# Optimization experiments

Measured on AMD Instinct MI355X. Metric: run time of the kernel, lower is better.

## Reference

```python
import jax, jax.numpy as jnp
import numpy as np

B, C, H, W = 8, 64, 128, 128


def _conv3x3(x, w, b):
    # x: [B,C,H,W], w: [O,I,3,3], b: [O]; stride 1, padding 1
    y = jax.lax.conv_general_dilated(
        x, w, window_strides=(1, 1), padding=((1, 1), (1, 1)),
        dimension_numbers=('NCHW', 'OIHW', 'NCHW'))
    return y + b[None, :, None, None]


def setup_inputs() -> dict:
    key = jax.random.key(0)
    ks = jax.random.split(key, 8)
    s = 0.05
    return {
        'x': jax.random.normal(ks[0], (B, C, H, W), jnp.float32),
        'Wq': jax.random.normal(ks[1], (C, C, 3, 3), jnp.float32) * s,
        'bq': jax.random.normal(ks[2], (C,), jnp.float32) * s,
        'Wk': jax.random.normal(ks[3], (C, C, 3, 3), jnp.float32) * s,
        'bk': jax.random.normal(ks[4], (C,), jnp.float32) * s,
        'Wv': jax.random.normal(ks[5], (C, C, 3, 3), jnp.float32) * s,
        'bv': jax.random.normal(ks[6], (C,), jnp.float32) * s,
        'gamma': jax.random.normal(ks[7], (1,), jnp.float32) * s,
    }


def reference(x, Wq, bq, Wk, bk, Wv, bv, gamma):
    b_, c_, h_, w_ = x.shape
    q = _conv3x3(x, Wq, bq)  # [B,C,H,W]
    k = _conv3x3(x, Wk, bk)
    v = _conv3x3(x, Wv, bv)

    # energy along H (column attention): eH[b,h,w,g] = sum_c q[b,c,h,w]*k[b,c,g,w]
    eH = jnp.einsum('bchw,bcgw->bhwg', q, k)
    eye = jnp.eye(h_, dtype=bool)  # mask diagonal h==g with -inf
    eH = jnp.where(eye[None, :, None, :], -jnp.inf, eH)

    # energy along W (row attention): eW[b,h,w,g] = sum_c q[b,c,h,w]*k[b,c,h,g]
    eW = jnp.einsum('bchw,bchg->bhwg', q, k)

    # joint softmax over concatenated [H | W] axis
    att = jax.nn.softmax(jnp.concatenate([eH, eW], axis=3), axis=3)
    att_H = att[:, :, :, :h_]          # [B,H,W,H]
    att_W = att[:, :, :, h_:h_ + w_]   # [B,H,W,W]

    out_H = jnp.einsum('bcgw,bhwg->bchw', v, att_H)
    out_W = jnp.einsum('bchg,bhwg->bchw', v, att_W)

    return gamma[0] * (out_H + out_W) + x
```

## Files before the change

### kernel.cpp

```cpp
#include <hip/hip_runtime.h>
#include <hip/hip_bf16.h>

#define B_ 8
#define C_ 64
#define H_ 128
#define W_ 128
#define HW_  ((size_t)H_ * W_)
#define CHW_ ((size_t)C_ * H_ * W_)

typedef unsigned short u16;
typedef unsigned int   u32;
typedef __attribute__((ext_vector_type(8))) short bf16x8;
typedef __attribute__((ext_vector_type(4))) float f32x4;

__device__ __forceinline__ float bf2f(u16 h) {
    union { u32 u; float f; } c; c.u = ((u32)h) << 16; return c.f;
}
__device__ __forceinline__ u16 f2bf(float f) {
    union { float f; u32 u; } c; c.f = f;
    u32 u = c.u;
    u32 r = (u + 0x7fffu + ((u >> 16) & 1u)) >> 16;
    return (u16)r;
}
__device__ __forceinline__ u32 pack2(float a, float b) {
    return (u32)f2bf(a) | ((u32)f2bf(b) << 16);
}
__device__ __forceinline__ float sanit(float x, float lo, float hi) {
    return fminf(fmaxf(x, lo), hi);
}
__device__ __forceinline__ void gload_lds16(const u16* g, u16* l) {
    __builtin_amdgcn_global_load_lds(
        (const __attribute__((address_space(1))) void*)g,
        (__attribute__((address_space(3))) void*)l, 16, 0, 0);
}

__global__ __launch_bounds__(256) void prep_weights(
    const float* __restrict__ Wq, const float* __restrict__ Wk,
    const float* __restrict__ Wv, u16* __restrict__ Wt)
{
    int tap = blockIdx.x;
    int cog = blockIdx.y * 4 + (threadIdx.x >> 6);
    int ci  = threadIdx.x & 63;
    int arr = cog >> 6, co = cog & 63;
    const float* src = arr == 0 ? Wq : (arr == 1 ? Wk : Wv);
    Wt[tap * 12288 + cog * 64 + ci] = f2bf(src[(co * 64 + ci) * 9 + tap]);
}

__global__ __launch_bounds__(256) void xprep_kernel(
    const float* __restrict__ x, u16* __restrict__ xb)
{
    const int hp  = blockIdx.x;
    const int tid = threadIdx.x;
    u16* dst = xb + ((size_t)blockIdx.y * 130 + hp) * 8192;
    if (hp == 0 || hp == 129) {
#pragma unroll
        for (int i = 0; i < 4; i++)
            *(uint4*)(dst + (size_t)(tid + i * 256) * 8) = (uint4){0, 0, 0, 0};
        return;
    }
    const float* xr = x + (size_t)blockIdx.y * CHW_ + (size_t)(hp - 1) * W_;
#pragma unroll
    for (int it = 0; it < 4; it++) {
        int idx = tid + it * 256;
        int px  = idx & 127;
        int g   = idx >> 7;
        float vb[8];
#pragma unroll
        for (int e = 0; e < 8; e++)
            vb[e] = xr[(size_t)(g * 8 + e) * HW_ + px];
        uint4 o;
        o.x = pack2(vb[0], vb[1]);
        o.y = pack2(vb[2], vb[3]);
        o.z = pack2(vb[4], vb[5]);
        o.w = pack2(vb[6], vb[7]);
        *(uint4*)(dst + (size_t)(g * 128 + px) * 8) = o;
    }
}

__global__ __launch_bounds__(256, 2) void conv_mfma_kernel(
    const u16* __restrict__ xb, const u16* __restrict__ Wt,
    const float* __restrict__ bq, const float* __restrict__ bk,
    const float* __restrict__ bv,
    u16* __restrict__ qN, u16* __restrict__ kN, u16* __restrict__ v)
{
    const int nwg  = gridDim.x * gridDim.y;
    const int flat = blockIdx.y * gridDim.x + blockIdx.x;
    const int wg   = (flat & 7) * (nwg >> 3) + (flat >> 3);
    const int h    = wg & (H_ - 1);
    const int bidx = wg >> 7;
    const size_t boff = (size_t)bidx * CHW_;
    const int tid  = threadIdx.x;
    const int lane = tid & 63, wv = tid >> 6;
    const int ln15 = lane & 15, quad = lane >> 4;

    __shared__ __align__(16) u16 xI[24960];

    const int woff = (wv * 48 + ln15) * 64 + quad * 8;

    bf16x8 wcur[2][3], wnxt[2][3];
#pragma unroll
    for (int ks = 0; ks < 2; ks++)
#pragma unroll
        for (int mt = 0; mt < 3; mt++)
            wcur[ks][mt] = *(const bf16x8*)(Wt + woff + mt * 1024 + ks * 32);

    if (tid < 48) {
        int dh = tid >> 4, g = (tid & 15) >> 1, p = (tid & 1) ? 129 : 0;
        *(uint4*)(xI + dh * 8320 + g * 1040 + p * 8) = (uint4){0, 0, 0, 0};
    }

    const u16* xrows = xb + ((size_t)bidx * 130 + h) * 8192;
#pragma unroll
    for (int it = 0; it < 12; it++) {
        int chunk = wv * 12 + it;
        int dh = chunk >> 4, g = (chunk >> 1) & 7, half = chunk & 1;
        gload_lds16(xrows + (size_t)dh * 8192 + g * 1024 + half * 512 + lane * 8,
                    xI + dh * 8320 + g * 1040 + 8 + half * 512);
    }
    __syncthreads();

    f32x4 acc[3][8];
#pragma unroll
    for (int mt = 0; mt < 3; mt++)
#pragma unroll
        for (int nt = 0; nt < 8; nt++)
            acc[mt][nt] = (f32x4){0.f, 0.f, 0.f, 0.f};

#pragma unroll
    for (int tap = 0; tap < 9; tap++) {
        const int dh = tap / 3, dw = tap % 3;
        if (tap < 8) {
#pragma unroll
            for (int ks = 0; ks < 2; ks++)
#pragma unroll
                for (int mt = 0; mt < 3; mt++)
                    wnxt[ks][mt] = *(const bf16x8*)(Wt + (tap + 1) * 12288 + woff + mt * 1024 + ks * 32);
        }
        const u16* xrow = xI + dh * 8320;
#pragma unroll
        for (int ks = 0; ks < 2; ks++) {
            bf16x8 bfr[8];
#pragma unroll
            for (int nt = 0; nt < 8; nt++)
                bfr[nt] = *(const bf16x8*)(xrow + ((quad + ks * 4) * 1040 + (nt * 16 + ln15 + dw) * 8));
            __builtin_amdgcn_s_setprio(1);
#pragma unroll
            for (int mt = 0; mt < 3; mt++)
#pragma unroll
                for (int nt = 0; nt < 8; nt++)
                    acc[mt][nt] = __builtin_amdgcn_mfma_f32_16x16x32_bf16(
                        wcur[ks][mt], bfr[nt], acc[mt][nt], 0, 0, 0);
            __builtin_amdgcn_s_setprio(0);
        }
        if (tap < 8) {
#pragma unroll
            for (int ks = 0; ks < 2; ks++)
#pragma unroll
                for (int mt = 0; mt < 3; mt++)
                    wcur[ks][mt] = wnxt[ks][mt];
        }
    }

    __syncthreads();
    u16* T = xI;
#pragma unroll
    for (int mt = 0; mt < 3; mt++) {
        int base = wv * 48 + mt * 16;
        int arr  = base >> 6;
        if (arr < 2) {
            const float* bias = arr == 0 ? bq : bk;
            int cb = (base & 63) + quad * 4;
#pragma unroll
            for (int r = 0; r < 4; r++) {
                float bb = bias[cb + r];
#pragma unroll
                for (int nt = 0; nt < 8; nt++)
                    T[arr * 9216 + (nt * 16 + ln15) * 72 + cb + r] = f2bf(acc[mt][nt][r] + bb);
            }
        } else {
            int cb = (base & 63) + quad * 4;
#pragma unroll
            for (int r = 0; r < 4; r++) {
                float bb = bv[cb + r];
                u16* drow = v + boff + (size_t)(cb + r) * HW_ + (size_t)h * W_;
#pragma unroll
                for (int nt = 0; nt < 8; nt++)
                    drow[nt * 16 + ln15] = f2bf(acc[mt][nt][r] + bb);
            }
        }
    }
    __syncthreads();
#pragma unroll
    for (int it = 0; it < 8; it++) {
        int idx = tid + it * 256;
        int arr = idx >> 10, rem = idx & 1023;
        int px = rem >> 3, c8 = (rem & 7) * 8;
        uint4 val = *(uint4*)(T + arr * 9216 + px * 72 + c8);
        u16* dst = (arr ? kN : qN) + boff + ((size_t)h * W_ + px) * 64 + c8;
        *(uint4*)dst = val;
    }
}

__global__ __launch_bounds__(256) void vt_kernel(
    const u16* __restrict__ v, u16* __restrict__ vT)
{
    __shared__ u16 Ts[64 * 72];
    const u16* src = v  + (size_t)blockIdx.z * CHW_ + (size_t)blockIdx.y * HW_;
    u16* dst       = vT + (size_t)blockIdx.z * CHW_ + (size_t)blockIdx.y * HW_;
    const int ti = blockIdx.x & 1, tj = blockIdx.x >> 1;
    const int r0 = ti * 64, c0 = tj * 64;
    const int tid = threadIdx.x;
    const int r = tid >> 2, cq = tid & 3;
#pragma unroll
    for (int i = 0; i < 2; i++) {
        uint4 u = *(const uint4*)(src + (size_t)(r0 + r) * 128 + c0 + cq * 16 + i * 8);
        *(uint4*)(Ts + r * 72 + cq * 16 + i * 8) = u;
    }
    __syncthreads();
    const int wr = tid >> 2, hq = tid & 3;
    union { u16 o[16]; uint4 v4[2]; } t;
#pragma unroll
    for (int j = 0; j < 16; j++) t.o[j] = Ts[(hq * 16 + j) * 72 + wr];
    *(uint4*)(dst + (size_t)(c0 + wr) * 128 + r0 + hq * 16)     = t.v4[0];
    *(uint4*)(dst + (size_t)(c0 + wr) * 128 + r0 + hq * 16 + 8) = t.v4[1];
}

__global__ __launch_bounds__(256, 3) void col_kernel(
    const u16* __restrict__ qN, const u16* __restrict__ kN,
    const u16* __restrict__ vT,
    float* __restrict__ maxH, float* __restrict__ sumH,
    float* __restrict__ Ocol)
{
    const size_t boff = (size_t)blockIdx.z * CHW_;
    const size_t soff = (size_t)blockIdx.z * HW_;
    qN += boff; kN += boff; vT += boff; Ocol += boff;
    maxH += soff; sumH += soff;

    const int s    = blockIdx.x;
    const int tid  = threadIdx.x;
    const int lane = tid & 63, wv = tid >> 6;
    const int ln15 = lane & 15, quad = lane >> 4;

    __shared__ __align__(16) u16 smemU[18432];
    u16* Qs = smemU;
    u16* Ks = smemU + 9216;

#pragma unroll
    for (int it = 0; it < 4; it++) {
        int idx = tid + it * 256;
        int t = idx >> 3, cg = (idx & 7) * 8;
        size_t off = (size_t)t * 8192 + (size_t)s * 64 + cg;
        *(uint4*)(Qs + t * 72 + cg) = *(const uint4*)(qN + off);
        *(uint4*)(Ks + t * 72 + cg) = *(const uint4*)(kN + off);
    }
    __syncthreads();

    f32x4 Sc[2][8];
#pragma unroll
    for (int mt = 0; mt < 2; mt++)
#pragma unroll
        for (int nt = 0; nt < 8; nt++)
            Sc[mt][nt] = (f32x4){0.f, 0.f, 0.f, 0.f};

#pragma unroll
    for (int ks = 0; ks < 2; ks++) {
        bf16x8 aq[2];
#pragma unroll
        for (int mt = 0; mt < 2; mt++)
            aq[mt] = *(const bf16x8*)(Qs + (wv * 32 + mt * 16 + ln15) * 72 + ks * 32 + quad * 8);
#pragma unroll
        for (int nt = 0; nt < 8; nt++) {
            bf16x8 bk_ = *(const bf16x8*)(Ks + (nt * 16 + ln15) * 72 + ks * 32 + quad * 8);
#pragma unroll
            for (int mt = 0; mt < 2; mt++)
                Sc[mt][nt] = __builtin_amdgcn_mfma_f32_16x16x32_bf16(aq[mt], bk_, Sc[mt][nt], 0, 0, 0);
        }
    }
#pragma unroll
    for (int mt = 0; mt < 2; mt++)
#pragma unroll
        for (int nt = 0; nt < 8; nt++)
#pragma unroll
            for (int r = 0; r < 4; r++) {
                int tt = wv * 32 + mt * 16 + quad * 4 + r;
                if (tt == nt * 16 + ln15) Sc[mt][nt][r] = -1e30f;
            }

    float mloc[2][4];
#pragma unroll
    for (int mt = 0; mt < 2; mt++)
#pragma unroll
        for (int r = 0; r < 4; r++) {
            float m = Sc[mt][0][r];
#pragma unroll
            for (int nt = 1; nt < 8; nt++) m = fmaxf(m, Sc[mt][nt][r]);
            for (int o = 1; o < 16; o <<= 1) m = fmaxf(m, __shfl_xor(m, o));
            float ss = 0.f;
#pragma unroll
            for (int nt = 0; nt < 8; nt++) ss += __expf(Sc[mt][nt][r] - m);
            for (int o = 1; o < 16; o <<= 1) ss += __shfl_xor(ss, o);
            mloc[mt][r] = m;
            if (ln15 == 0) {
                int tt = wv * 32 + mt * 16 + quad * 4 + r;
                int pix = tt * W_ + s;
                maxH[pix] = m; sumH[pix] = ss;
            }
        }
    __syncthreads();
    u16* Ps = smemU;
#pragma unroll
    for (int mt = 0; mt < 2; mt++)
#pragma unroll
        for (int nt = 0; nt < 8; nt++)
#pragma unroll
            for (int r = 0; r < 4; r++)
                Ps[(wv * 32 + mt * 16 + quad * 4 + r) * 136 + nt * 16 + ln15] =
                    f2bf(__expf(Sc[mt][nt][r] - mloc[mt][r]));
    __syncthreads();

    f32x4 Oc[2][4];
#pragma unroll
    for (int mt = 0; mt < 2; mt++)
#pragma unroll
        for (int nt = 0; nt < 4; nt++)
            Oc[mt][nt] = (f32x4){0.f, 0.f, 0.f, 0.f};
#pragma unroll
    for (int kg = 0; kg < 4; kg++) {
        bf16x8 ap[2];
#pragma unroll
        for (int mt = 0; mt < 2; mt++)
            ap[mt] = *(const bf16x8*)(Ps + (wv * 32 + mt * 16 + ln15) * 136 + kg * 32 + quad * 8);
#pragma unroll
        for (int nt = 0; nt < 4; nt++) {
            bf16x8 bv_ = *(const bf16x8*)(vT + (size_t)(nt * 16 + ln15) * HW_ + (size_t)s * 128 + kg * 32 + quad * 8);
#pragma unroll
            for (int mt = 0; mt < 2; mt++)
                Oc[mt][nt] = __builtin_amdgcn_mfma_f32_16x16x32_bf16(ap[mt], bv_, Oc[mt][nt], 0, 0, 0);
        }
    }
    __syncthreads();
    float* Of = (float*)smemU;
#pragma unroll
    for (int mt = 0; mt < 2; mt++)
#pragma unroll
        for (int nt = 0; nt < 4; nt++)
#pragma unroll
            for (int r = 0; r < 4; r++)
                Of[(wv * 32 + mt * 16 + quad * 4 + r) * 68 + nt * 16 + ln15] = Oc[mt][nt][r];
    __syncthreads();
#pragma unroll
    for (int it = 0; it < 8; it++) {
        int idx = tid + it * 256;
        int t = idx >> 4, c4 = (idx & 15) * 4;
        *(float4*)(Ocol + ((size_t)t * 128 + s) * 64 + c4) = *(float4*)(Of + t * 68 + c4);
    }
}

__global__ __launch_bounds__(256, 3) void row_kernel(
    const u16* __restrict__ qN, const u16* __restrict__ kN,
    const u16* __restrict__ v,
    const float* __restrict__ x, const float* __restrict__ gammap,
    const float* __restrict__ maxH, const float* __restrict__ sumH,
    const float* __restrict__ Ocol, float* __restrict__ out)
{
    const size_t boff = (size_t)blockIdx.z * CHW_;
    const size_t soff = (size_t)blockIdx.z * HW_;
    qN += boff; kN += boff; v += boff; Ocol += boff; x += boff; out += boff;
    maxH += soff; sumH += soff;

    const int s    = blockIdx.x;
    const int tid  = threadIdx.x;
    const int lane = tid & 63, wv = tid >> 6;
    const int ln15 = lane & 15, quad = lane >> 4;

    __shared__ __align__(16) u16 smemU[18432];
    u16* Qs = smemU;
    u16* Ks = smemU + 9216;

#pragma unroll
    for (int it = 0; it < 4; it++) {
        int idx = tid + it * 256;
        int t = idx >> 3, cg = (idx & 7) * 8;
        size_t off = (size_t)s * 8192 + (size_t)t * 64 + cg;
        *(uint4*)(Qs + t * 72 + cg) = *(const uint4*)(qN + off);
        *(uint4*)(Ks + t * 72 + cg) = *(const uint4*)(kN + off);
    }
    __syncthreads();

    f32x4 Sc[2][8];
#pragma unroll
    for (int mt = 0; mt < 2; mt++)
#pragma unroll
        for (int nt = 0; nt < 8; nt++)
            Sc[mt][nt] = (f32x4){0.f, 0.f, 0.f, 0.f};
#pragma unroll
    for (int ks = 0; ks < 2; ks++) {
        bf16x8 aq[2];
#pragma unroll
        for (int mt = 0; mt < 2; mt++)
            aq[mt] = *(const bf16x8*)(Qs + (wv * 32 + mt * 16 + ln15) * 72 + ks * 32 + quad * 8);
#pragma unroll
        for (int nt = 0; nt < 8; nt++) {
            bf16x8 bk_ = *(const bf16x8*)(Ks + (nt * 16 + ln15) * 72 + ks * 32 + quad * 8);
#pragma unroll
            for (int mt = 0; mt < 2; mt++)
                Sc[mt][nt] = __builtin_amdgcn_mfma_f32_16x16x32_bf16(aq[mt], bk_, Sc[mt][nt], 0, 0, 0);
        }
    }

    float mr[2][4], rr[2][4], al[2][4];
#pragma unroll
    for (int mt = 0; mt < 2; mt++)
#pragma unroll
        for (int r = 0; r < 4; r++) {
            float m = Sc[mt][0][r];
#pragma unroll
            for (int nt = 1; nt < 8; nt++) m = fmaxf(m, Sc[mt][nt][r]);
            for (int o = 1; o < 16; o <<= 1) m = fmaxf(m, __shfl_xor(m, o));
            float ss = 0.f;
#pragma unroll
            for (int nt = 0; nt < 8; nt++) ss += __expf(Sc[mt][nt][r] - m);
            for (int o = 1; o < 16; o <<= 1) ss += __shfl_xor(ss, o);
            int tt  = wv * 32 + mt * 16 + quad * 4 + r;
            int pix = s * W_ + tt;
            float mc = sanit(maxH[pix], -3e38f, 3e38f);
            float sc = sanit(sumH[pix], 0.f, 3e38f);
            float mm = fmaxf(mc, m);
            float dd = sc * __expf(fminf(mc - mm, 0.f)) + ss * __expf(fminf(m - mm, 0.f));
            float rv = 1.0f / fmaxf(dd, 1e-30f);
            mr[mt][r] = mm; rr[mt][r] = rv;
            al[mt][r] = __expf(fminf(mc - mm, 0.f)) * rv;
        }
    __syncthreads();
    u16* Ps = smemU;
#pragma unroll
    for (int mt = 0; mt < 2; mt++)
#pragma unroll
        for (int nt = 0; nt < 8; nt++)
#pragma unroll
            for (int r = 0; r < 4; r++)
                Ps[(wv * 32 + mt * 16 + quad * 4 + r) * 136 + nt * 16 + ln15] =
                    f2bf(__expf(fminf(Sc[mt][nt][r] - mr[mt][r], 0.f)) * rr[mt][r]);
    __syncthreads();

    f32x4 Oc[2][4];
#pragma unroll
    for (int mt = 0; mt < 2; mt++)
#pragma unroll
        for (int nt = 0; nt < 4; nt++)
            Oc[mt][nt] = (f32x4){0.f, 0.f, 0.f, 0.f};
#pragma unroll
    for (int kg = 0; kg < 4; kg++) {
        bf16x8 ap[2];
#pragma unroll
        for (int mt = 0; mt < 2; mt++)
            ap[mt] = *(const bf16x8*)(Ps + (wv * 32 + mt * 16 + ln15) * 136 + kg * 32 + quad * 8);
#pragma unroll
        for (int nt = 0; nt < 4; nt++) {
            bf16x8 bv_ = *(const bf16x8*)(v + (size_t)(nt * 16 + ln15) * HW_ + (size_t)s * 128 + kg * 32 + quad * 8);
#pragma unroll
            for (int mt = 0; mt < 2; mt++)
                Oc[mt][nt] = __builtin_amdgcn_mfma_f32_16x16x32_bf16(ap[mt], bv_, Oc[mt][nt], 0, 0, 0);
        }
    }
    __syncthreads();

    const float gmm = gammap[0];
    float* Of = (float*)smemU;
#pragma unroll
    for (int mt = 0; mt < 2; mt++)
#pragma unroll
        for (int nt = 0; nt < 4; nt++) {
            float fv[4];
            int c = nt * 16 + ln15;
#pragma unroll
            for (int r = 0; r < 4; r++) {
                int tt = wv * 32 + mt * 16 + quad * 4 + r;
                float oc = Ocol[((size_t)s * 128 + tt) * 64 + c];
                fv[r] = gmm * (Oc[mt][nt][r] + al[mt][r] * oc);
            }
            int w0 = wv * 32 + mt * 16 + quad * 4;
            *(float4*)(Of + c * 132 + w0) = make_float4(fv[0], fv[1], fv[2], fv[3]);
        }
    __syncthreads();
    int c = tid >> 2, w0 = (tid & 3) * 32;
#pragma unroll
    for (int i = 0; i < 8; i++) {
        int w = w0 + i * 4;
        float4 xo = *(const float4*)(x + (size_t)c * HW_ + (size_t)s * 128 + w);
        float4 of = *(const float4*)(Of + c * 132 + w);
        *(float4*)(out + (size_t)c * HW_ + (size_t)s * 128 + w) =
            make_float4(of.x + xo.x, of.y + xo.y, of.z + xo.z, of.w + xo.w);
    }
}

extern "C" void kernel_launch(void* const* d_in, const int* in_sizes, int n_in,
                              void* d_out, int out_size, void* d_ws, size_t ws_size,
                              hipStream_t stream)
{
    const float* x  = (const float*)d_in[0];
    const float* Wq = (const float*)d_in[1];
    const float* bq = (const float*)d_in[2];
    const float* Wk = (const float*)d_in[3];
    const float* bk = (const float*)d_in[4];
    const float* Wv = (const float*)d_in[5];
    const float* bv = (const float*)d_in[6];
    const float* gm = (const float*)d_in[7];
    float* out = (float*)d_out;

    char* ws = (char*)d_ws;
    const size_t need1 = 4 * (size_t)B_ * CHW_ * 2 + (size_t)B_ * CHW_ * 4
                       + 2 * (size_t)B_ * HW_ * 4 + 221184;
    int passes = (ws_size >= need1) ? 1 : 2;
    int nb = B_ / passes;

    const size_t SL = (size_t)nb * CHW_ * 2;
    const size_t OC = (size_t)nb * CHW_ * 4;
    const size_t ST = (size_t)nb * HW_ * 4;
    u16*   qNb  = (u16*)(ws);
    u16*   kNb  = (u16*)(ws + SL);
    u16*   v    = (u16*)(ws + 2 * SL);
    u16*   vT   = (u16*)(ws + 3 * SL);
    float* Ocol = (float*)(ws + 4 * SL);
    float* maxH = (float*)(ws + 4 * SL + OC);
    float* sumH = (float*)(ws + 4 * SL + OC + ST);
    u16*   Wt   = (u16*)(ws + 4 * SL + OC + 2 * ST);
    u16*   xb   = (u16*)Ocol;

    dim3 blk(256);
    prep_weights<<<dim3(9, 48), blk, 0, stream>>>(Wq, Wk, Wv, Wt);

    for (int p = 0; p < passes; p++) {
        const float* xbp = x + (size_t)p * nb * CHW_;
        float* ob = out + (size_t)p * nb * CHW_;
        xprep_kernel<<<dim3(130, nb), blk, 0, stream>>>(xbp, xb);
        conv_mfma_kernel<<<dim3(H_, nb), blk, 0, stream>>>(xb, Wt, bq, bk, bv, qNb, kNb, v);
        vt_kernel<<<dim3(4, C_, nb), blk, 0, stream>>>(v, vT);
        col_kernel<<<dim3(W_, 1, nb), blk, 0, stream>>>(qNb, kNb, vT, maxH, sumH, Ocol);
        row_kernel<<<dim3(H_, 1, nb), blk, 0, stream>>>(qNb, kNb, v, xbp, gm, maxH, sumH, Ocol, ob);
    }
}
```

Baseline: 198.6 us.

## Store conv q/k directly from registers, cache exponentials, prefetch column stats

The conv kernel's per-wave output-channel mapping is changed so each wave owns 16 channels of each of q, k and v. Each lane can then write packed q/k values straight to global memory, dropping the LDS transpose stage and its two barriers. Both attention kernels keep the softmax exponentials in registers instead of recomputing expf when writing P, and the row kernel loads the column max/sum before the QK compute. The trade-off is narrower, strided 8-byte global stores instead of coalesced 16-byte ones, plus added register pressure from the cached values.

```diff
diff --git a/kernel.cpp b/kernel.cpp
--- a/kernel.cpp
+++ b/kernel.cpp
@@ -95,14 +95,14 @@
 
     __shared__ __align__(16) u16 xI[24960];
 
-    const int woff = (wv * 48 + ln15) * 64 + quad * 8;
+    const int woff = (wv * 16 + ln15) * 64 + quad * 8;
 
     bf16x8 wcur[2][3], wnxt[2][3];
 #pragma unroll
     for (int ks = 0; ks < 2; ks++)
 #pragma unroll
         for (int mt = 0; mt < 3; mt++)
-            wcur[ks][mt] = *(const bf16x8*)(Wt + woff + mt * 1024 + ks * 32);
+            wcur[ks][mt] = *(const bf16x8*)(Wt + woff + mt * 4096 + ks * 32);
 
     if (tid < 48) {
         int dh = tid >> 4, g = (tid & 15) >> 1, p = (tid & 1) ? 129 : 0;
@@ -134,7 +134,7 @@
             for (int ks = 0; ks < 2; ks++)
 #pragma unroll
                 for (int mt = 0; mt < 3; mt++)
-                    wnxt[ks][mt] = *(const bf16x8*)(Wt + (tap + 1) * 12288 + woff + mt * 1024 + ks * 32);
+                    wnxt[ks][mt] = *(const bf16x8*)(Wt + (tap + 1) * 12288 + woff + mt * 4096 + ks * 32);
         }
         const u16* xrow = xI + dh * 8320;
 #pragma unroll
@@ -161,43 +161,31 @@
         }
     }
 
-    __syncthreads();
-    u16* T = xI;
+    const int cb = wv * 16 + quad * 4;
 #pragma unroll
     for (int mt = 0; mt < 3; mt++) {
-        int base = wv * 48 + mt * 16;
-        int arr  = base >> 6;
-        if (arr < 2) {
-            const float* bias = arr == 0 ? bq : bk;
-            int cb = (base & 63) + quad * 4;
+        const float* bias = mt == 0 ? bq : (mt == 1 ? bk : bv);
+        float b0 = bias[cb], b1 = bias[cb + 1], b2 = bias[cb + 2], b3 = bias[cb + 3];
+        if (mt < 2) {
+            u16* dst = (mt ? kN : qN) + boff + (size_t)h * W_ * 64 + cb;
+#pragma unroll
+            for (int nt = 0; nt < 8; nt++) {
+                int px = nt * 16 + ln15;
+                u32 p0 = pack2(acc[mt][nt][0] + b0, acc[mt][nt][1] + b1);
+                u32 p1 = pack2(acc[mt][nt][2] + b2, acc[mt][nt][3] + b3);
+                *(u32*)(dst + (size_t)px * 64)     = p0;
+                *(u32*)(dst + (size_t)px * 64 + 2) = p1;
+            }
+        } else {
+            float bb[4] = {b0, b1, b2, b3};
 #pragma unroll
             for (int r = 0; r < 4; r++) {
-                float bb = bias[cb + r];
+                u16* drow = v + boff + (size_t)(cb + r) * HW_ + (size_t)h * W_;
 #pragma unroll
                 for (int nt = 0; nt < 8; nt++)
-                    T[arr * 9216 + (nt * 16 + ln15) * 72 + cb + r] = f2bf(acc[mt][nt][r] + bb);
-            }
-        } else {
-            int cb = (base & 63) + quad * 4;
-#pragma unroll
-            for (int r = 0; r < 4; r++) {
-                float bb = bv[cb + r];
-                u16* drow = v + boff + (size_t)(cb + r) * HW_ + (size_t)h * W_;
-#pragma unroll
-                for (int nt = 0; nt < 8; nt++)
-                    drow[nt * 16 + ln15] = f2bf(acc[mt][nt][r] + bb);
-            }
-        }
-    }
-    __syncthreads();
-#pragma unroll
-    for (int it = 0; it < 8; it++) {
-        int idx = tid + it * 256;
-        int arr = idx >> 10, rem = idx & 1023;
-        int px = rem >> 3, c8 = (rem & 7) * 8;
-        uint4 val = *(uint4*)(T + arr * 9216 + px * 72 + c8);
-        u16* dst = (arr ? kN : qN) + boff + ((size_t)h * W_ + px) * 64 + c8;
-        *(uint4*)dst = val;
+                    drow[nt * 16 + ln15] = f2bf(acc[mt][nt][r] + bb[r]);
+            }
+        }
     }
 }
 
@@ -286,7 +274,6 @@
                 if (tt == nt * 16 + ln15) Sc[mt][nt][r] = -1e30f;
             }
 
-    float mloc[2][4];
 #pragma unroll
     for (int mt = 0; mt < 2; mt++)
 #pragma unroll
@@ -297,9 +284,12 @@
             for (int o = 1; o < 16; o <<= 1) m = fmaxf(m, __shfl_xor(m, o));
             float ss = 0.f;
 #pragma unroll
-            for (int nt = 0; nt < 8; nt++) ss += __expf(Sc[mt][nt][r] - m);
+            for (int nt = 0; nt < 8; nt++) {
+                float e = __expf(Sc[mt][nt][r] - m);
+                ss += e;
+                Sc[mt][nt][r] = e;
+            }
             for (int o = 1; o < 16; o <<= 1) ss += __shfl_xor(ss, o);
-            mloc[mt][r] = m;
             if (ln15 == 0) {
                 int tt = wv * 32 + mt * 16 + quad * 4 + r;
                 int pix = tt * W_ + s;
@@ -315,7 +305,7 @@
 #pragma unroll
             for (int r = 0; r < 4; r++)
                 Ps[(wv * 32 + mt * 16 + quad * 4 + r) * 136 + nt * 16 + ln15] =
-                    f2bf(__expf(Sc[mt][nt][r] - mloc[mt][r]));
+                    f2bf(Sc[mt][nt][r]);
     __syncthreads();
 
     f32x4 Oc[2][4];
@@ -377,6 +367,16 @@
     u16* Qs = smemU;
     u16* Ks = smemU + 9216;
 
+    float mcv[2][4], scv[2][4];
+#pragma unroll
+    for (int mt = 0; mt < 2; mt++)
+#pragma unroll
+        for (int r = 0; r < 4; r++) {
+            int tt = wv * 32 + mt * 16 + quad * 4 + r;
+            mcv[mt][r] = maxH[s * W_ + tt];
+            scv[mt][r] = sumH[s * W_ + tt];
+        }
+
 #pragma unroll
     for (int it = 0; it < 4; it++) {
         int idx = tid + it * 256;
@@ -408,7 +408,7 @@
         }
     }
 
-    float mr[2][4], rr[2][4], al[2][4];
+    float be[2][4], al[2][4];
 #pragma unroll
     for (int mt = 0; mt < 2; mt++)
 #pragma unroll
@@ -419,16 +419,18 @@
             for (int o = 1; o < 16; o <<= 1) m = fmaxf(m, __shfl_xor(m, o));
             float ss = 0.f;
 #pragma unroll
-            for (int nt = 0; nt < 8; nt++) ss += __expf(Sc[mt][nt][r] - m);
+            for (int nt = 0; nt < 8; nt++) {
+                float e = __expf(Sc[mt][nt][r] - m);
+                ss += e;
+                Sc[mt][nt][r] = e;
+            }
             for (int o = 1; o < 16; o <<= 1) ss += __shfl_xor(ss, o);
-            int tt  = wv * 32 + mt * 16 + quad * 4 + r;
-            int pix = s * W_ + tt;
-            float mc = sanit(maxH[pix], -3e38f, 3e38f);
-            float sc = sanit(sumH[pix], 0.f, 3e38f);
+            float mc = sanit(mcv[mt][r], -3e38f, 3e38f);
+            float sc = sanit(scv[mt][r], 0.f, 3e38f);
             float mm = fmaxf(mc, m);
-            float dd = sc * __expf(fminf(mc - mm, 0.f)) + ss * __expf(fminf(m - mm, 0.f));
+            float dd = sc * __expf(fminf(mc - mm, 0.f)) + ss * __expf(m - mm);
             float rv = 1.0f / fmaxf(dd, 1e-30f);
-            mr[mt][r] = mm; rr[mt][r] = rv;
+            be[mt][r] = __expf(m - mm) * rv;
             al[mt][r] = __expf(fminf(mc - mm, 0.f)) * rv;
         }
     __syncthreads();
@@ -440,7 +442,7 @@
 #pragma unroll
             for (int r = 0; r < 4; r++)
                 Ps[(wv * 32 + mt * 16 + quad * 4 + r) * 136 + nt * 16 + ln15] =
-                    f2bf(__expf(fminf(Sc[mt][nt][r] - mr[mt][r], 0.f)) * rr[mt][r]);
+                    f2bf(Sc[mt][nt][r] * be[mt][r]);
     __syncthreads();
 
     f32x4 Oc[2][4];
```

After: 198.5 us. No clear change (-0.0%).
